# Performance work log

Hardware: AMD Instinct MI355X
Metric: run time of the kernel (lower is better)

## Reference

```python
import jax, jax.numpy as jnp
import numpy as np

B, L, D = 2, 2048, 1024
H = 16
HD = D // H            # 64
HALF = HD // 2         # 32
PHASE_SCALE = 1.0
SCALE = HD ** -0.5


def _orthogonal_projection(rng, d, m):
    g = rng.standard_normal((d, m)).astype(np.float32)
    q, r = np.linalg.qr(g)
    s = np.sign(np.diagonal(r))
    s = np.where(s == 0, 1.0, s).astype(np.float32)
    q = q * s[None, :]
    q = q * np.sqrt(d / m)  # preserve_variance=True
    return jnp.asarray(q)


def setup_inputs() -> dict:
    key = jax.random.key(0)
    ks = jax.random.split(key, 6)
    rng = np.random.default_rng(0)
    return {
        "x": jax.random.normal(ks[0], (B, L, D), dtype=jnp.float32),
        "p": jax.random.normal(ks[1], (B, L, D), dtype=jnp.float32),
        "Wqkv": jax.random.normal(ks[2], (D, 3 * D), dtype=jnp.float32) * (D ** -0.5),
        "bqkv": jax.random.normal(ks[3], (3 * D,), dtype=jnp.float32) * 0.02,
        "Wout": jax.random.normal(ks[4], (D, D), dtype=jnp.float32) * (D ** -0.5),
        "bout": jax.random.normal(ks[5], (D,), dtype=jnp.float32) * 0.02,
        "proj": _orthogonal_projection(rng, D, D // 2),
    }


def _rotate_half(t, cos, sin):
    # non-interleaved rotary: split head_dim in halves
    t1, t2 = t[..., :HALF], t[..., HALF:]
    return jnp.concatenate((t1 * cos - t2 * sin, t1 * sin + t2 * cos), axis=-1)


def reference(x, p, Wqkv, bqkv, Wout, bout, proj):
    Bx, Lx = x.shape[0], x.shape[1]
    # QKV projection -> (B, L, 3, H, HD)
    qkv = (x @ Wqkv + bqkv).reshape(Bx, Lx, 3, H, HD)
    q, k, v = qkv[:, :, 0], qkv[:, :, 1], qkv[:, :, 2]
    # collaborative rotary phases from conditioning tokens p
    phases = (p @ proj).reshape(Bx, Lx, H, HALF) * PHASE_SCALE
    cos, sin = jnp.cos(phases), jnp.sin(phases)
    q = _rotate_half(q, cos, sin)
    k = _rotate_half(k, cos, sin)
    # non-causal softmax attention, scale = head_dim^-0.5
    scores = jnp.einsum("blhd,bmhd->bhlm", q, k) * SCALE
    attn = jax.nn.softmax(scores, axis=-1)
    out = jnp.einsum("bhlm,bmhd->blhd", attn, v).reshape(Bx, Lx, D)
    return out @ Wout + bout
```

## Files before the change

kernel.cpp:

```cpp
#include <hip/hip_runtime.h>


typedef __bf16 bf16;
typedef __bf16 bf16x8 __attribute__((ext_vector_type(8)));
typedef __bf16 bf16x4 __attribute__((ext_vector_type(4)));
typedef float f32x4 __attribute__((ext_vector_type(4)));
typedef float f32x16 __attribute__((ext_vector_type(16)));
typedef unsigned int u32;

__device__ __forceinline__ bf16 f2bf(float f) {
  unsigned u = __builtin_bit_cast(unsigned, f);
  u += 0x7FFFu + ((u >> 16) & 1u);
  unsigned short h = (unsigned short)(u >> 16);
  return __builtin_bit_cast(bf16, h);
}

__device__ __forceinline__ void gload_lds16(const bf16* g, bf16* l) {
  __builtin_amdgcn_global_load_lds((const __attribute__((address_space(1))) u32*)(const void*)g,
                                   (__attribute__((address_space(3))) u32*)(void*)l, 16, 0, 0);
}

__device__ __forceinline__ u32 cvtpk_bf16(float lo, float hi) {
  u32 r;
  asm("v_cvt_pk_bf16_f32 %0, %1, %2" : "=v"(r) : "v"(lo), "v"(hi));
  return r;
}
__device__ __forceinline__ void perm32swap(u32& a, u32& b) {
  asm("v_permlane32_swap_b32 %0, %1" : "+v"(a), "+v"(b));
}

#if __has_builtin(__builtin_amdgcn_exp2f)
#define EXP2(x) __builtin_amdgcn_exp2f(x)
#else
#define EXP2(x) exp2f(x)
#endif

#define QSCALE 0.18033688f

__device__ __forceinline__ void xcd_remap(int& bx, int& by) {
  const int nx = gridDim.x;
  const int nwg = nx * gridDim.y;
  const int lin = blockIdx.y * nx + blockIdx.x;
  const int chunk = nwg >> 3;
  const int nid = (lin & 7) * chunk + (lin >> 3);
  bx = nid % nx;
  by = nid / nx;
}

__global__ __launch_bounds__(256) void k_prep(const float* __restrict__ x, bf16* __restrict__ xb,
                                              const float* __restrict__ p, bf16* __restrict__ pb,
                                              const float* __restrict__ W1, bf16* __restrict__ O1,
                                              const float* __restrict__ W2, bf16* __restrict__ O2,
                                              const float* __restrict__ W3, bf16* __restrict__ O3) {
  const int gb = blockIdx.x;
  if (gb < 8192) {
    int i = gb * 256 + threadIdx.x;
    const float* in = x; bf16* out = xb;
    if (i >= 1048576) { in = p; out = pb; i -= 1048576; }
    const float4 v = ((const float4*)in)[i];
    bf16x4 o;
    o[0] = f2bf(v.x); o[1] = f2bf(v.y); o[2] = f2bf(v.z); o[3] = f2bf(v.w);
    *(bf16x4*)(out + (size_t)i * 4) = o;
    return;
  }
  __shared__ float t[64][65];
  const int lin = gb - 8192;
  int bx = lin % 72;
  const int by = lin / 72;
  const float* in; bf16* out; int C;
  if (bx < 48)      { in = W1; out = O1; C = 3072; }
  else if (bx < 56) { in = W2; out = O2; C = 512;  bx -= 48; }
  else              { in = W3; out = O3; C = 1024; bx -= 56; }
  const int R = 1024;
  const int c0 = bx * 64, r0 = by * 64;
  for (int e = threadIdx.x; e < 4096; e += 256) {
    int r = e >> 6, c = e & 63;
    t[r][c] = in[(size_t)(r0 + r) * C + c0 + c];
  }
  __syncthreads();
  for (int e = threadIdx.x; e < 4096; e += 256) {
    int c = e >> 6, r = e & 63;
    out[(size_t)(c0 + c) * R + r0 + r] = f2bf(t[r][c]);
  }
}

__global__ __launch_bounds__(512, 4) void k_gemm128x64(const bf16* __restrict__ A,
                                                       const bf16* __restrict__ Bt,
                                                       const float* __restrict__ bias,
                                                       float* __restrict__ C,
                                                       int M, int N, int K) {
  __shared__ bf16 sA0[8192], sA1[8192];
  __shared__ bf16 sB0[4096], sB1[4096];
  const int tid = threadIdx.x;
  const int lane = tid & 63, w = tid >> 6;
  const int lrow = lane & 15, lgrp = lane >> 4;
  const int wm = (w >> 1) * 32, wn = (w & 1) * 32;
  int bx, by;
  xcd_remap(bx, by);
  const int m0 = bx * 128, n0 = by * 64;
  const int srow = tid >> 3;
  const int swz8 = ((tid & 7) ^ (srow & 7)) * 8;
  const int r7 = lrow & 7;
  const int nkt = K >> 6;

  const bf16* Ab = A  + (size_t)m0 * K;
  const bf16* Bb = Bt + (size_t)n0 * K;

  f32x4 acc[2][2] = {};

#pragma unroll
  for (int c = 0; c < 2; ++c)
    gload_lds16(Ab + (size_t)(c * 64 + srow) * K + swz8, sA0 + c * 4096 + w * 512);
  gload_lds16(Bb + (size_t)srow * K + swz8, sB0 + w * 512);
  __syncthreads();

  for (int kt = 0; kt < nkt; ++kt) {
    const bf16* pA = (kt & 1) ? sA1 : sA0;
    const bf16* pB = (kt & 1) ? sB1 : sB0;
    bf16* nA = (kt & 1) ? sA0 : sA1;
    bf16* nB = (kt & 1) ? sB0 : sB1;
    const size_t knext = (size_t)(kt + 1) * 64;

    if (kt < nkt - 1) {
#pragma unroll
      for (int c = 0; c < 2; ++c)
        gload_lds16(Ab + (size_t)(c * 64 + srow) * K + knext + swz8, nA + c * 4096 + w * 512);
      gload_lds16(Bb + (size_t)srow * K + knext + swz8, nB + w * 512);
    }

#pragma unroll
    for (int kk = 0; kk < 2; ++kk) {
      bf16x8 af[2], bfr[2];
#pragma unroll
      for (int mi = 0; mi < 2; ++mi)
        af[mi] = *(const bf16x8*)&pA[(wm + mi * 16 + lrow) * 64 + ((kk * 4 + lgrp) ^ r7) * 8];
#pragma unroll
      for (int ni = 0; ni < 2; ++ni)
        bfr[ni] = *(const bf16x8*)&pB[(wn + ni * 16 + lrow) * 64 + ((kk * 4 + lgrp) ^ r7) * 8];
      __builtin_amdgcn_s_setprio(1);
#pragma unroll
      for (int mi = 0; mi < 2; ++mi)
#pragma unroll
        for (int ni = 0; ni < 2; ++ni)
          acc[mi][ni] = __builtin_amdgcn_mfma_f32_16x16x32_bf16(af[mi], bfr[ni], acc[mi][ni], 0, 0, 0);
      __builtin_amdgcn_s_setprio(0);
    }
    __syncthreads();
  }

#pragma unroll
  for (int mi = 0; mi < 2; ++mi)
#pragma unroll
    for (int ni = 0; ni < 2; ++ni) {
      const int col = n0 + wn + ni * 16 + lrow;
      const float bv = bias ? bias[col] : 0.f;
#pragma unroll
      for (int j = 0; j < 4; ++j) {
        const int row = m0 + wm + mi * 16 + lgrp * 4 + j;
        C[(size_t)row * N + col] = acc[mi][ni][j] + bv;
      }
    }
}

__global__ __launch_bounds__(512, 2) void k_gemm_qkv256(const bf16* __restrict__ A,
                                                        const bf16* __restrict__ Bt,
                                                        const float* __restrict__ bqkv,
                                                        const float* __restrict__ phases,
                                                        bf16* __restrict__ qb,
                                                        bf16* __restrict__ kb,
                                                        bf16* __restrict__ vb) {
  __shared__ bf16 sA0[16384], sA1[16384];
  __shared__ bf16 sB0[16384], sB1[16384];
  const int tid = threadIdx.x;
  const int lane = tid & 63, w = tid >> 6;
  const int lrow = lane & 15, lgrp = lane >> 4;
  const int wm = (w >> 2) * 128;
  const int wn = (w & 3) * 64;
  const int m0 = blockIdx.x * 256, n0 = blockIdx.y * 256;
  const int K = 1024;

  const int srow = tid >> 3;
  const int swz8 = (((tid & 7) ^ (srow & 7))) * 8;
  const int r7 = lrow & 7;

  const bf16* Ab = A  + (size_t)m0 * K;
  const bf16* Bb = Bt + (size_t)n0 * K;

  f32x4 acc[8][4] = {};

#pragma unroll
  for (int g = 0; g < 4; ++g) {
    gload_lds16(Ab + (size_t)(g * 64 + srow) * K + swz8, sA0 + g * 4096 + w * 512);
    gload_lds16(Bb + (size_t)(g * 64 + srow) * K + swz8, sB0 + g * 4096 + w * 512);
  }
  __syncthreads();

  for (int kt = 0; kt < 16; ++kt) {
    const bf16* pA = (kt & 1) ? sA1 : sA0;
    const bf16* pB = (kt & 1) ? sB1 : sB0;
    bf16* nA = (kt & 1) ? sA0 : sA1;
    bf16* nB = (kt & 1) ? sB0 : sB1;
    const size_t knext = (size_t)(kt + 1) * 64;

    if (kt < 15) {
#pragma unroll
      for (int g = 0; g < 4; ++g) {
        gload_lds16(Ab + (size_t)(g * 64 + srow) * K + knext + swz8, nA + g * 4096 + w * 512);
        gload_lds16(Bb + (size_t)(g * 64 + srow) * K + knext + swz8, nB + g * 4096 + w * 512);
      }
    }

    bf16x8 bfr[4][2];
#pragma unroll
    for (int ni = 0; ni < 4; ++ni)
#pragma unroll
      for (int kk = 0; kk < 2; ++kk)
        bfr[ni][kk] = *(const bf16x8*)&pB[(wn + ni * 16 + lrow) * 64 + ((kk * 4 + lgrp) ^ r7) * 8];

#pragma unroll
    for (int q = 0; q < 4; ++q) {
      bf16x8 af[2][2];
#pragma unroll
      for (int m2 = 0; m2 < 2; ++m2)
#pragma unroll
        for (int kk = 0; kk < 2; ++kk)
          af[m2][kk] = *(const bf16x8*)&pA[(wm + (q * 2 + m2) * 16 + lrow) * 64 + ((kk * 4 + lgrp) ^ r7) * 8];
      __builtin_amdgcn_s_setprio(1);
#pragma unroll
      for (int m2 = 0; m2 < 2; ++m2)
#pragma unroll
        for (int ni = 0; ni < 4; ++ni)
#pragma unroll
          for (int kk = 0; kk < 2; ++kk)
            acc[q * 2 + m2][ni] =
                __builtin_amdgcn_mfma_f32_16x16x32_bf16(af[m2][kk], bfr[ni][kk], acc[q * 2 + m2][ni], 0, 0, 0);
      __builtin_amdgcn_s_setprio(0);
    }
    __syncthreads();
  }

  const int nw = n0 + wn;
  const int sec = nw >> 10;
  const int hh = (nw & 1023) >> 6;
  const float b0 = bqkv[nw + lrow];
  const float b1 = bqkv[nw + 16 + lrow];
  const float b2 = bqkv[nw + 32 + lrow];
  const float b3 = bqkv[nw + 48 + lrow];

  if (sec == 2) {
#pragma unroll
    for (int mi = 0; mi < 8; ++mi) {
      const int row0 = m0 + wm + mi * 16 + lgrp * 4;
      const int b = row0 >> 11, l0 = row0 & 2047;
#pragma unroll
      for (int ni = 0; ni < 4; ++ni) {
        const int d = ni * 16 + lrow;
        const float bv = (ni == 0) ? b0 : (ni == 1) ? b1 : (ni == 2) ? b2 : b3;
        bf16x4 pv;
#pragma unroll
        for (int j = 0; j < 4; ++j) pv[j] = f2bf(acc[mi][ni][j] + bv);
        *(bf16x4*)&vb[(((size_t)(b * 16 + hh)) * 64 + d) * 2048 + l0] = pv;
      }
    }
  } else {
    bf16* qk = sec ? kb : qb;
    const float qs = sec ? 1.0f : QSCALE;
#pragma unroll
    for (int mi = 0; mi < 8; ++mi) {
#pragma unroll
      for (int j = 0; j < 4; ++j) {
        const int row = m0 + wm + mi * 16 + lgrp * 4 + j;
        const int b = row >> 11, l = row & 2047;
        const float ph1 = phases[(size_t)row * 512 + hh * 32 + lrow];
        const float ph2 = phases[(size_t)row * 512 + hh * 32 + 16 + lrow];
        float s1, c1, s2, c2;
        __sincosf(ph1, &s1, &c1);
        __sincosf(ph2, &s2, &c2);
        const float t0 = acc[mi][0][j] + b0;
        const float t1 = acc[mi][1][j] + b1;
        const float t2 = acc[mi][2][j] + b2;
        const float t3 = acc[mi][3][j] + b3;
        bf16* base = qk + (((size_t)(b * 16 + hh)) * 2048 + l) * 64;
        base[lrow]      = f2bf((t0 * c1 - t2 * s1) * qs);
        base[16 + lrow] = f2bf((t1 * c2 - t3 * s2) * qs);
        base[32 + lrow] = f2bf((t0 * s1 + t2 * c1) * qs);
        base[48 + lrow] = f2bf((t1 * s2 + t3 * c2) * qs);
      }
    }
  }
}

__global__ __launch_bounds__(512, 4) void k_flash_attn11(const bf16* __restrict__ qb,
                                                         const bf16* __restrict__ kb,
                                                         const bf16* __restrict__ vb,
                                                         bf16* __restrict__ attnout) {
  const int tid = threadIdx.x, lane = tid & 63, w = tid >> 6;
  const int ql = lane & 31, hi = lane >> 5;
  const int qgrp = w >> 2;
  const int tsel = (w >> 1) & 1;
  const int qh = w & 1;
  const int fid = blockIdx.x;
  const int nid = (fid & 7) * 64 + (fid >> 3);
  const int qblk = nid & 15, h = (nid >> 4) & 15, b = nid >> 8;
  const size_t bh = (size_t)b * 16 + h;
  const bf16* Kp = kb + bh * 2048 * 64;
  const bf16* Vp = vb + bh * 64 * 2048;

  __shared__ __align__(16) char smem[40960];
  bf16* sKb[3] = { (bf16*)smem, (bf16*)(smem + 8192), (bf16*)(smem + 16384) };
  bf16* sVb[2] = { (bf16*)(smem + 24576), (bf16*)(smem + 32768) };

  const bf16* Qp = qb + (bh * 2048 + (size_t)qblk * 128 + qgrp * 64 + qh * 32 + ql) * 64;
  bf16x8 qf[4];
#pragma unroll
  for (int c = 0; c < 4; ++c) qf[c] = *(const bf16x8*)(Qp + c * 16 + hi * 8);

  const int srow = tid >> 3;
  const int swz = (tid & 7) ^ (srow & 7);
  const int jk0 = (0 * 2 + hi) ^ (ql & 7), jk1 = (1 * 2 + hi) ^ (ql & 7);
  const int jk2 = (2 * 2 + hi) ^ (ql & 7), jk3 = (3 * 2 + hi) ^ (ql & 7);
  const int jv0 = (tsel * 4 + 0 + hi) ^ (ql & 7);
  const int jv1 = (tsel * 4 + 2 + hi) ^ (ql & 7);
  const int krow = (tsel * 32 + ql) * 64;

  f32x16 o0 = {}, o1 = {};
  float lsum = 0.f;
  u32 pcu[8];
  bf16x8 vfr[4];
  bf16x8 kfn[4];

#define STAGE_K(PTR, KV0)                                                               \
  gload_lds16(Kp + (size_t)((KV0) + srow) * 64 + swz * 8, (PTR) + w * 512)
#define STAGE_V(PTR, KV0)                                                               \
  gload_lds16(Vp + (size_t)srow * 2048 + (KV0) + swz * 8, (PTR) + w * 512)

#define KF_PREFETCH(PTR)                                       \
  do {                                                         \
    kfn[0] = *(const bf16x8*)&(PTR)[krow + jk0 * 8];           \
    kfn[1] = *(const bf16x8*)&(PTR)[krow + jk1 * 8];           \
    kfn[2] = *(const bf16x8*)&(PTR)[krow + jk2 * 8];           \
    kfn[3] = *(const bf16x8*)&(PTR)[krow + jk3 * 8];           \
  } while (0)

#define SM_PACK(VPTR)                                                               \
  do {                                                                              \
    _Pragma("unroll")                                                               \
    for (int j2 = 0; j2 < 16; ++j2) {                                               \
      float pv = EXP2(st0[j2]);                                                     \
      st0[j2] = pv; lsum += pv;                                                     \
    }                                                                               \
    {                                                                               \
      u32 a0 = cvtpk_bf16(st0[0], st0[1]),  a1 = cvtpk_bf16(st0[2], st0[3]);        \
      u32 a2 = cvtpk_bf16(st0[4], st0[5]),  a3 = cvtpk_bf16(st0[6], st0[7]);        \
      perm32swap(a0, a2); perm32swap(a1, a3);                                       \
      pcu[0] = a0; pcu[1] = a1; pcu[2] = a2; pcu[3] = a3;                           \
      u32 b0 = cvtpk_bf16(st0[8], st0[9]),  b1 = cvtpk_bf16(st0[10], st0[11]);      \
      u32 b2 = cvtpk_bf16(st0[12], st0[13]), b3 = cvtpk_bf16(st0[14], st0[15]);     \
      perm32swap(b0, b2); perm32swap(b1, b3);                                       \
      pcu[4] = b0; pcu[5] = b1; pcu[6] = b2; pcu[7] = b3;                           \
    }                                                                               \
    vfr[0] = *(const bf16x8*)&(VPTR)[ql * 64 + jv0 * 8];                            \
    vfr[1] = *(const bf16x8*)&(VPTR)[(32 + ql) * 64 + jv0 * 8];                     \
    vfr[2] = *(const bf16x8*)&(VPTR)[ql * 64 + jv1 * 8];                            \
    vfr[3] = *(const bf16x8*)&(VPTR)[(32 + ql) * 64 + jv1 * 8];                     \
  } while (0)

#define PV_PREV()                                                                   \
  do {                                                                              \
    union { u32 u[4]; bf16x8 v; } cA, cB;                                           \
    cA.u[0] = pcu[0]; cA.u[1] = pcu[1]; cA.u[2] = pcu[2]; cA.u[3] = pcu[3];         \
    cB.u[0] = pcu[4]; cB.u[1] = pcu[5]; cB.u[2] = pcu[6]; cB.u[3] = pcu[7];         \
    __builtin_amdgcn_s_setprio(1);                                                  \
    o0 = __builtin_amdgcn_mfma_f32_32x32x16_bf16(vfr[0], cA.v, o0, 0, 0, 0);        \
    o1 = __builtin_amdgcn_mfma_f32_32x32x16_bf16(vfr[1], cA.v, o1, 0, 0, 0);        \
    o0 = __builtin_amdgcn_mfma_f32_32x32x16_bf16(vfr[2], cB.v, o0, 0, 0, 0);        \
    o1 = __builtin_amdgcn_mfma_f32_32x32x16_bf16(vfr[3], cB.v, o1, 0, 0, 0);        \
    __builtin_amdgcn_s_setprio(0);                                                  \
  } while (0)

  bf16 *ka = sKb[0], *kbuf = sKb[1], *kc = sKb[2];
  bf16 *va = sVb[0], *vbuf = sVb[1];

  STAGE_K(ka, 0);
  STAGE_K(kbuf, 64);
  STAGE_V(va, 0);
  __syncthreads();

  {
    STAGE_K(kc, 128);
    STAGE_V(vbuf, 64);
    f32x16 st0 = {};
    bf16x8 kf0 = *(const bf16x8*)&ka[krow + jk0 * 8];
    bf16x8 kf1 = *(const bf16x8*)&ka[krow + jk1 * 8];
    bf16x8 kf2 = *(const bf16x8*)&ka[krow + jk2 * 8];
    bf16x8 kf3 = *(const bf16x8*)&ka[krow + jk3 * 8];
    __builtin_amdgcn_s_setprio(1);
    st0 = __builtin_amdgcn_mfma_f32_32x32x16_bf16(kf0, qf[0], st0, 0, 0, 0);
    st0 = __builtin_amdgcn_mfma_f32_32x32x16_bf16(kf1, qf[1], st0, 0, 0, 0);
    st0 = __builtin_amdgcn_mfma_f32_32x32x16_bf16(kf2, qf[2], st0, 0, 0, 0);
    st0 = __builtin_amdgcn_mfma_f32_32x32x16_bf16(kf3, qf[3], st0, 0, 0, 0);
    __builtin_amdgcn_s_setprio(0);
    KF_PREFETCH(kbuf);
    SM_PACK(va);
    __syncthreads();
    bf16* tmp = ka; ka = kbuf; kbuf = kc; kc = tmp;
    bf16* tv = va; va = vbuf; vbuf = tv;
  }

  for (int t = 1; t < 32; ++t) {
    if (t < 31) {
      STAGE_V(vbuf, (t + 1) * 64);
      if (t < 30) STAGE_K(kc, (t + 2) * 64);
    }
    f32x16 st0 = {};
    __builtin_amdgcn_s_setprio(1);
    st0 = __builtin_amdgcn_mfma_f32_32x32x16_bf16(kfn[0], qf[0], st0, 0, 0, 0);
    st0 = __builtin_amdgcn_mfma_f32_32x32x16_bf16(kfn[1], qf[1], st0, 0, 0, 0);
    st0 = __builtin_amdgcn_mfma_f32_32x32x16_bf16(kfn[2], qf[2], st0, 0, 0, 0);
    st0 = __builtin_amdgcn_mfma_f32_32x32x16_bf16(kfn[3], qf[3], st0, 0, 0, 0);
    __builtin_amdgcn_s_setprio(0);
    PV_PREV();
    if (t < 31) KF_PREFETCH(kbuf);
    SM_PACK(va);
    __syncthreads();
    bf16* tmp = ka; ka = kbuf; kbuf = kc; kc = tmp;
    bf16* tv = va; va = vbuf; vbuf = tv;
  }

  PV_PREV();

  float* cb = (float*)smem;
  if (tsel == 1) {
    const int idx = ((qgrp * 2 + qh) * 64 + lane) * 34;
#pragma unroll
    for (int i = 0; i < 16; ++i) cb[idx + i] = o0[i];
#pragma unroll
    for (int i = 0; i < 16; ++i) cb[idx + 16 + i] = o1[i];
    cb[idx + 32] = lsum;
  }
  __syncthreads();
  if (tsel == 0) {
    const int idx = ((qgrp * 2 + qh) * 64 + lane) * 34;
#pragma unroll
    for (int i = 0; i < 16; ++i) o0[i] += cb[idx + i];
#pragma unroll
    for (int i = 0; i < 16; ++i) o1[i] += cb[idx + 16 + i];
    lsum += cb[idx + 32];
    lsum += __shfl_xor(lsum, 32);

    const float inv = 1.f / lsum;
    const int qrow = qblk * 128 + qgrp * 64 + qh * 32 + ql;
    bf16* outp = attnout + ((size_t)b * 2048 + qrow) * 1024 + h * 64;
#pragma unroll
    for (int j2 = 0; j2 < 4; ++j2) {
      bf16x4 ov;
#pragma unroll
      for (int jj = 0; jj < 4; ++jj) ov[jj] = f2bf(o0[j2 * 4 + jj] * inv);
      *(bf16x4*)(outp + j2 * 8 + hi * 4) = ov;
#pragma unroll
      for (int jj = 0; jj < 4; ++jj) ov[jj] = f2bf(o1[j2 * 4 + jj] * inv);
      *(bf16x4*)(outp + 32 + j2 * 8 + hi * 4) = ov;
    }
  }
#undef STAGE_K
#undef STAGE_V
#undef KF_PREFETCH
#undef SM_PACK
#undef PV_PREV
}

extern "C" void kernel_launch(void* const* d_in, const int* in_sizes, int n_in,
                              void* d_out, int out_size, void* d_ws, size_t ws_size,
                              hipStream_t stream) {
  (void)in_sizes; (void)n_in; (void)out_size; (void)ws_size;
  const float* x    = (const float*)d_in[0];
  const float* p    = (const float*)d_in[1];
  const float* Wqkv = (const float*)d_in[2];
  const float* bqkv = (const float*)d_in[3];
  const float* Wout = (const float*)d_in[4];
  const float* bout = (const float*)d_in[5];
  const float* proj = (const float*)d_in[6];
  float* out = (float*)d_out;

  char* ws = (char*)d_ws;
  size_t off = 0;
  bf16* xb     = (bf16*)(ws + off); off += (size_t)4096 * 1024 * 2;
  bf16* pb     = (bf16*)(ws + off); off += (size_t)4096 * 1024 * 2;
  bf16* WqkvT  = (bf16*)(ws + off); off += (size_t)3072 * 1024 * 2;
  bf16* projT  = (bf16*)(ws + off); off += (size_t)512  * 1024 * 2;
  bf16* WoutT  = (bf16*)(ws + off); off += (size_t)1024 * 1024 * 2;
  float* phases= (float*)(ws + off); off += (size_t)4096 * 512 * 4;
  bf16* qb     = (bf16*)(ws + off); off += (size_t)4096 * 1024 * 2;
  bf16* kb     = (bf16*)(ws + off); off += (size_t)4096 * 1024 * 2;
  bf16* vb     = (bf16*)(ws + off); off += (size_t)4096 * 1024 * 2;
  bf16* attnb  = (bf16*)(ws + off); off += (size_t)4096 * 1024 * 2;

  k_prep<<<9344, 256, 0, stream>>>(x, xb, p, pb, Wqkv, WqkvT, proj, projT, Wout, WoutT);

  k_gemm128x64<<<dim3(32, 8), 512, 0, stream>>>(pb, projT, nullptr, phases, 4096, 512, 1024);
  k_gemm_qkv256<<<dim3(16, 12), 512, 0, stream>>>(xb, WqkvT, bqkv, phases, qb, kb, vb);

  k_flash_attn11<<<512, 512, 0, stream>>>(qb, kb, vb, attnb);

  k_gemm128x64<<<dim3(32, 16), 512, 0, stream>>>(attnb, WoutT, bout, out, 4096, 1024, 1024);
}
```

Measured before the change: 122.5 us.

## Stage K/V in 128-key super-tiles with double buffering to halve barriers

The attention kernel now stages K and V in 128-key super-tiles (two 64-key subtiles each) with plain double buffering. This replaces the triple-buffered K and double-buffered V rotation with its per-64-key barrier, so a block synchronizes 16 times instead of 32. Two QK/softmax/PV subtiles run between barriers, and the register prefetch of K fragments from the next tile is removed. LDS per block grows from 40 KB to 64 KB, which may reduce how many blocks fit on a CU. K-fragment LDS loads are also no longer hidden behind the previous iteration's work.

Result: no change. 123.9 us (+1.1%).

```diff
diff --git a/kernel.cpp b/kernel.cpp
--- a/kernel.cpp
+++ b/kernel.cpp
@@ -290,7 +290,7 @@
   }
 }
 
-__global__ __launch_bounds__(512, 4) void k_flash_attn11(const bf16* __restrict__ qb,
+__global__ __launch_bounds__(512, 4) void k_flash_attn13(const bf16* __restrict__ qb,
                                                          const bf16* __restrict__ kb,
                                                          const bf16* __restrict__ vb,
                                                          bf16* __restrict__ attnout) {
@@ -306,9 +306,9 @@
   const bf16* Kp = kb + bh * 2048 * 64;
   const bf16* Vp = vb + bh * 64 * 2048;
 
-  __shared__ __align__(16) char smem[40960];
-  bf16* sKb[3] = { (bf16*)smem, (bf16*)(smem + 8192), (bf16*)(smem + 16384) };
-  bf16* sVb[2] = { (bf16*)(smem + 24576), (bf16*)(smem + 32768) };
+  __shared__ __align__(16) char smem[65536];
+  bf16* sK = (bf16*)smem;
+  bf16* sV = (bf16*)(smem + 32768);
 
   const bf16* Qp = qb + (bh * 2048 + (size_t)qblk * 128 + qgrp * 64 + qh * 32 + ql) * 64;
   bf16x8 qf[4];
@@ -327,22 +327,30 @@
   float lsum = 0.f;
   u32 pcu[8];
   bf16x8 vfr[4];
-  bf16x8 kfn[4];
-
-#define STAGE_K(PTR, KV0)                                                               \
-  gload_lds16(Kp + (size_t)((KV0) + srow) * 64 + swz * 8, (PTR) + w * 512)
-#define STAGE_V(PTR, KV0)                                                               \
-  gload_lds16(Vp + (size_t)srow * 2048 + (KV0) + swz * 8, (PTR) + w * 512)
-
-#define KF_PREFETCH(PTR)                                       \
-  do {                                                         \
-    kfn[0] = *(const bf16x8*)&(PTR)[krow + jk0 * 8];           \
-    kfn[1] = *(const bf16x8*)&(PTR)[krow + jk1 * 8];           \
-    kfn[2] = *(const bf16x8*)&(PTR)[krow + jk2 * 8];           \
-    kfn[3] = *(const bf16x8*)&(PTR)[krow + jk3 * 8];           \
+
+#define STAGE_SUPER(KPTR, VPTR, KV0)                                                       \
+  do {                                                                                     \
+    gload_lds16(Kp + (size_t)((KV0) + srow) * 64 + swz * 8,      (KPTR) + w * 512);        \
+    gload_lds16(Kp + (size_t)((KV0) + 64 + srow) * 64 + swz * 8, (KPTR) + 4096 + w * 512); \
+    gload_lds16(Vp + (size_t)srow * 2048 + (KV0) + swz * 8,        (VPTR) + w * 512);      \
+    gload_lds16(Vp + (size_t)srow * 2048 + (KV0) + 64 + swz * 8,   (VPTR) + 4096 + w * 512); \
   } while (0)
 
-#define SM_PACK(VPTR)                                                               \
+#define KF_QK(KSUB)                                                                \
+  do {                                                                             \
+    bf16x8 kf0 = *(const bf16x8*)&(KSUB)[krow + jk0 * 8];                          \
+    bf16x8 kf1 = *(const bf16x8*)&(KSUB)[krow + jk1 * 8];                          \
+    bf16x8 kf2 = *(const bf16x8*)&(KSUB)[krow + jk2 * 8];                          \
+    bf16x8 kf3 = *(const bf16x8*)&(KSUB)[krow + jk3 * 8];                          \
+    __builtin_amdgcn_s_setprio(1);                                                 \
+    st0 = __builtin_amdgcn_mfma_f32_32x32x16_bf16(kf0, qf[0], st0, 0, 0, 0);       \
+    st0 = __builtin_amdgcn_mfma_f32_32x32x16_bf16(kf1, qf[1], st0, 0, 0, 0);       \
+    st0 = __builtin_amdgcn_mfma_f32_32x32x16_bf16(kf2, qf[2], st0, 0, 0, 0);       \
+    st0 = __builtin_amdgcn_mfma_f32_32x32x16_bf16(kf3, qf[3], st0, 0, 0, 0);       \
+    __builtin_amdgcn_s_setprio(0);                                                 \
+  } while (0)
+
+#define SM_PACK(VSUB)                                                               \
   do {                                                                              \
     _Pragma("unroll")                                                               \
     for (int j2 = 0; j2 < 16; ++j2) {                                               \
@@ -359,10 +367,10 @@
       perm32swap(b0, b2); perm32swap(b1, b3);                                       \
       pcu[4] = b0; pcu[5] = b1; pcu[6] = b2; pcu[7] = b3;                           \
     }                                                                               \
-    vfr[0] = *(const bf16x8*)&(VPTR)[ql * 64 + jv0 * 8];                            \
-    vfr[1] = *(const bf16x8*)&(VPTR)[(32 + ql) * 64 + jv0 * 8];                     \
-    vfr[2] = *(const bf16x8*)&(VPTR)[ql * 64 + jv1 * 8];                            \
-    vfr[3] = *(const bf16x8*)&(VPTR)[(32 + ql) * 64 + jv1 * 8];                     \
+    vfr[0] = *(const bf16x8*)&(VSUB)[ql * 64 + jv0 * 8];                            \
+    vfr[1] = *(const bf16x8*)&(VSUB)[(32 + ql) * 64 + jv0 * 8];                     \
+    vfr[2] = *(const bf16x8*)&(VSUB)[ql * 64 + jv1 * 8];                            \
+    vfr[3] = *(const bf16x8*)&(VSUB)[(32 + ql) * 64 + jv1 * 8];                     \
   } while (0)
 
 #define PV_PREV()                                                                   \
@@ -378,53 +386,48 @@
     __builtin_amdgcn_s_setprio(0);                                                  \
   } while (0)
 
-  bf16 *ka = sKb[0], *kbuf = sKb[1], *kc = sKb[2];
-  bf16 *va = sVb[0], *vbuf = sVb[1];
-
-  STAGE_K(ka, 0);
-  STAGE_K(kbuf, 64);
-  STAGE_V(va, 0);
+  STAGE_SUPER(sK, sV, 0);
   __syncthreads();
 
   {
-    STAGE_K(kc, 128);
-    STAGE_V(vbuf, 64);
-    f32x16 st0 = {};
-    bf16x8 kf0 = *(const bf16x8*)&ka[krow + jk0 * 8];
-    bf16x8 kf1 = *(const bf16x8*)&ka[krow + jk1 * 8];
-    bf16x8 kf2 = *(const bf16x8*)&ka[krow + jk2 * 8];
-    bf16x8 kf3 = *(const bf16x8*)&ka[krow + jk3 * 8];
-    __builtin_amdgcn_s_setprio(1);
-    st0 = __builtin_amdgcn_mfma_f32_32x32x16_bf16(kf0, qf[0], st0, 0, 0, 0);
-    st0 = __builtin_amdgcn_mfma_f32_32x32x16_bf16(kf1, qf[1], st0, 0, 0, 0);
-    st0 = __builtin_amdgcn_mfma_f32_32x32x16_bf16(kf2, qf[2], st0, 0, 0, 0);
-    st0 = __builtin_amdgcn_mfma_f32_32x32x16_bf16(kf3, qf[3], st0, 0, 0, 0);
-    __builtin_amdgcn_s_setprio(0);
-    KF_PREFETCH(kbuf);
-    SM_PACK(va);
+    STAGE_SUPER(sK + 8192, sV + 8192, 128);
+    const bf16* kcur = sK;
+    const bf16* vcur = sV;
+    {
+      f32x16 st0 = {};
+      KF_QK(kcur);
+      SM_PACK(vcur);
+    }
+    {
+      f32x16 st0 = {};
+      KF_QK(kcur + 4096);
+      PV_PREV();
+      SM_PACK(vcur + 4096);
+    }
     __syncthreads();
-    bf16* tmp = ka; ka = kbuf; kbuf = kc; kc = tmp;
-    bf16* tv = va; va = vbuf; vbuf = tv;
-  }
-
-  for (int t = 1; t < 32; ++t) {
-    if (t < 31) {
-      STAGE_V(vbuf, (t + 1) * 64);
-      if (t < 30) STAGE_K(kc, (t + 2) * 64);
-    }
-    f32x16 st0 = {};
-    __builtin_amdgcn_s_setprio(1);
-    st0 = __builtin_amdgcn_mfma_f32_32x32x16_bf16(kfn[0], qf[0], st0, 0, 0, 0);
-    st0 = __builtin_amdgcn_mfma_f32_32x32x16_bf16(kfn[1], qf[1], st0, 0, 0, 0);
-    st0 = __builtin_amdgcn_mfma_f32_32x32x16_bf16(kfn[2], qf[2], st0, 0, 0, 0);
-    st0 = __builtin_amdgcn_mfma_f32_32x32x16_bf16(kfn[3], qf[3], st0, 0, 0, 0);
-    __builtin_amdgcn_s_setprio(0);
-    PV_PREV();
-    if (t < 31) KF_PREFETCH(kbuf);
-    SM_PACK(va);
+  }
+
+  for (int t = 1; t < 16; ++t) {
+    bf16* kcur = sK + (t & 1) * 8192;
+    bf16* vcur = sV + (t & 1) * 8192;
+    if (t < 15) {
+      bf16* knxt = sK + ((t + 1) & 1) * 8192;
+      bf16* vnxt = sV + ((t + 1) & 1) * 8192;
+      STAGE_SUPER(knxt, vnxt, (t + 1) * 128);
+    }
+    {
+      f32x16 st0 = {};
+      KF_QK(kcur);
+      PV_PREV();
+      SM_PACK(vcur);
+    }
+    {
+      f32x16 st0 = {};
+      KF_QK(kcur + 4096);
+      PV_PREV();
+      SM_PACK(vcur + 4096);
+    }
     __syncthreads();
-    bf16* tmp = ka; ka = kbuf; kbuf = kc; kc = tmp;
-    bf16* tv = va; va = vbuf; vbuf = tv;
   }
 
   PV_PREV();
@@ -462,9 +465,8 @@
       *(bf16x4*)(outp + 32 + j2 * 8 + hi * 4) = ov;
     }
   }
-#undef STAGE_K
-#undef STAGE_V
-#undef KF_PREFETCH
+#undef STAGE_SUPER
+#undef KF_QK
 #undef SM_PACK
 #undef PV_PREV
 }
@@ -500,7 +502,7 @@
   k_gemm128x64<<<dim3(32, 8), 512, 0, stream>>>(pb, projT, nullptr, phases, 4096, 512, 1024);
   k_gemm_qkv256<<<dim3(16, 12), 512, 0, stream>>>(xb, WqkvT, bqkv, phases, qb, kb, vb);
 
-  k_flash_attn11<<<512, 512, 0, stream>>>(qb, kb, vb, attnb);
+  k_flash_attn13<<<512, 512, 0, stream>>>(qb, kb, vb, attnb);
 
   k_gemm128x64<<<dim3(32, 16), 512, 0, stream>>>(attnb, WoutT, bout, out, 4096, 1024, 1024);
 }
```
